# Kernel optimization log

Measured on AMD Instinct MI355X. Metric: run time of the kernel, lower is better.

The kernel has to match this reference:

```python
import jax, jax.numpy as jnp
import numpy as np

HIDDEN = 896
N_HEADS = 14
N_KV_HEADS = 2
HEAD_DIM = HIDDEN // N_HEADS  # 64
KV_GROUPS = N_HEADS // N_KV_HEADS  # 7
ROPE_THETA = 1000000.0


def rotate_half(x):
    x1, x2 = x[..., : x.shape[-1] // 2], x[..., x.shape[-1] // 2 :]
    return jnp.concatenate((-x2, x1), axis=-1)


def rope_tables(seq_len, dtype=jnp.float32):
    inv_freq = 1.0 / (ROPE_THETA ** (jnp.arange(0, HEAD_DIM, 2, dtype=jnp.float32) / HEAD_DIM))
    t = jnp.arange(seq_len, dtype=jnp.float32)
    freqs = jnp.outer(t, inv_freq)            # [S, D/2]
    emb = jnp.concatenate((freqs, freqs), -1)  # [S, D]
    return jnp.cos(emb).astype(dtype), jnp.sin(emb).astype(dtype)


def setup_inputs() -> dict:
    key = jax.random.key(0)
    ks = jax.random.split(key, 8)
    B, S = 2, 2048
    s = 0.02
    return {
        "hidden_states": jax.random.normal(ks[0], (B, S, HIDDEN), jnp.float32),
        "wq": jax.random.normal(ks[1], (HIDDEN, N_HEADS * HEAD_DIM), jnp.float32) * s,
        "bq": jnp.zeros((N_HEADS * HEAD_DIM,), jnp.float32),
        "wk": jax.random.normal(ks[2], (HIDDEN, N_KV_HEADS * HEAD_DIM), jnp.float32) * s,
        "bk": jnp.zeros((N_KV_HEADS * HEAD_DIM,), jnp.float32),
        "wv": jax.random.normal(ks[3], (HIDDEN, N_KV_HEADS * HEAD_DIM), jnp.float32) * s,
        "bv": jnp.zeros((N_KV_HEADS * HEAD_DIM,), jnp.float32),
        "wo": jax.random.normal(ks[4], (N_HEADS * HEAD_DIM, HIDDEN), jnp.float32) * s,
    }


def reference(hidden_states, wq, bq, wk, bk, wv, bv, wo):
    B, S, _ = hidden_states.shape
    q = (hidden_states @ wq + bq).reshape(B, S, N_HEADS, HEAD_DIM)
    k = (hidden_states @ wk + bk).reshape(B, S, N_KV_HEADS, HEAD_DIM)
    v = (hidden_states @ wv + bv).reshape(B, S, N_KV_HEADS, HEAD_DIM)

    cos, sin = rope_tables(S, hidden_states.dtype)
    cos, sin = cos[None, :, None, :], sin[None, :, None, :]
    q = q * cos + rotate_half(q) * sin
    k = k * cos + rotate_half(k) * sin

    # GQA broadcast: repeat kv heads to match query heads
    k = jnp.repeat(k, KV_GROUPS, axis=2)
    v = jnp.repeat(v, KV_GROUPS, axis=2)

    # [B, H, S, S]
    scores = jnp.einsum("bqhd,bkhd->bhqk", q, k) / jnp.sqrt(jnp.asarray(HEAD_DIM, hidden_states.dtype))
    mask = jnp.tril(jnp.ones((S, S), dtype=jnp.bool_))
    scores = jnp.where(mask[None, None, :, :], scores, jnp.asarray(-1e9, scores.dtype))
    attn = jax.nn.softmax(scores, axis=-1)
    out = jnp.einsum("bhqk,bkhd->bqhd", attn, v).reshape(B, S, N_HEADS * HEAD_DIM)
    return out @ wo
```

## Files before the change

kernel.cpp:

```cpp
#include <hip/hip_runtime.h>

#define HID 896
#define NQ 896
#define NKV 128
#define NQKV 1152
#define NH 14
#define NKVH 2
#define GQ 7
#define DH 64
#define SEQ 2048
#define BATCH 2
#define TOK (BATCH*SEQ)

typedef __attribute__((ext_vector_type(8))) short short8;
typedef __attribute__((ext_vector_type(4))) float f32x4;
typedef __attribute__((ext_vector_type(4))) unsigned short us4;

__device__ __forceinline__ unsigned short f2bf(float x) {
  unsigned int u = __builtin_bit_cast(unsigned int, x);
  u = (u + 0x7fffu + ((u >> 16) & 1u)) >> 16;
  return (unsigned short)u;
}
__device__ __forceinline__ float bf2f(unsigned short b) {
  return __builtin_bit_cast(float, (unsigned int)b << 16);
}
__device__ __forceinline__ f32x4 fzero4() {
  f32x4 z; z[0]=0.f; z[1]=0.f; z[2]=0.f; z[3]=0.f; return z;
}
__device__ __forceinline__ unsigned int cvt_pk_bf16(float lo, float hi) {
  unsigned int r;
  asm("v_cvt_pk_bf16_f32 %0, %1, %2" : "=v"(r) : "v"(lo), "v"(hi));
  return r;
}
__device__ __forceinline__ void gload_lds16(const unsigned short* g, unsigned short* l) {
  __builtin_amdgcn_global_load_lds(
      (const __attribute__((address_space(1))) void*)(const void*)g,
      (__attribute__((address_space(3))) void*)(void*)l, 16, 0, 0);
}

#define CVT_BLKS 3584
#define TRN_BLKS 448
#define BIAS_BLKS 5
#define TAB_BLKS 256
#define PREP_BLKS (CVT_BLKS + TRN_BLKS + BIAS_BLKS + TAB_BLKS)

__global__ void k_prep(const float* __restrict__ hs,
                       const float* __restrict__ wq, const float* __restrict__ bq,
                       const float* __restrict__ wk, const float* __restrict__ bk,
                       const float* __restrict__ wv, const float* __restrict__ bv,
                       const float* __restrict__ wo,
                       unsigned short* __restrict__ hb,
                       unsigned short* __restrict__ wqkvt,
                       unsigned short* __restrict__ wot,
                       float* __restrict__ bqkv,
                       float2* __restrict__ cs) {
  __shared__ unsigned short Ls[64*65];
  int blk = blockIdx.x, tid = threadIdx.x;
  if (blk < CVT_BLKS) {
    int i = blk*256 + tid;
    float4 v = ((const float4*)hs)[i];
    us4 o; o[0]=f2bf(v.x); o[1]=f2bf(v.y); o[2]=f2bf(v.z); o[3]=f2bf(v.w);
    ((us4*)hb)[i] = o;
    return;
  }
  blk -= CVT_BLKS;
  if (blk < TRN_BLKS) {
    const float* W; unsigned short* out; int K, N, n0, k0;
    if (blk < 196)      { W=wq; out=wqkvt;                        K=HID; N=NQ;  int t=blk;     n0=(t%14)*64; k0=(t/14)*64; }
    else if (blk < 224) { W=wk; out=wqkvt + (size_t)NQ*HID;       K=HID; N=NKV; int t=blk-196; n0=(t%2)*64;  k0=(t/2)*64; }
    else if (blk < 252) { W=wv; out=wqkvt + (size_t)(NQ+NKV)*HID; K=HID; N=NKV; int t=blk-224; n0=(t%2)*64;  k0=(t/2)*64; }
    else                { W=wo; out=wot;                          K=NQ;  N=HID; int t=blk-252; n0=(t%14)*64; k0=(t/14)*64; }
    #pragma unroll
    for (int i = 0; i < 16; ++i) {
      int idx = i*256 + tid;
      int r = idx >> 6, c = idx & 63;
      Ls[c*65 + r] = f2bf(W[(size_t)(k0 + r)*N + n0 + c]);
    }
    __syncthreads();
    #pragma unroll
    for (int i = 0; i < 16; ++i) {
      int idx = i*256 + tid;
      int r2 = idx >> 6, c2 = idx & 63;
      out[(size_t)(n0 + r2)*K + k0 + c2] = Ls[r2*65 + c2];
    }
    return;
  }
  blk -= TRN_BLKS;
  if (blk < BIAS_BLKS) {
    int i = blk*256 + tid;
    if (i < NQKV) {
      if (i < NQ) bqkv[i] = bq[i];
      else if (i < NQ + NKV) bqkv[i] = bk[i - NQ];
      else bqkv[i] = bv[i - NQ - NKV];
    }
    return;
  }
  blk -= BIAS_BLKS;
  {
    int i = blk*256 + tid;
    int s = i >> 5, dp = i & 31;
    float inv = __expf(-(float)(2*dp) * (13.815510557964274f / 64.0f));
    float f = (float)s * inv;
    cs[i] = make_float2(cosf(f), sinf(f));
  }
}

template<int OUTMODE>
__global__ __launch_bounds__(256, 3) void k_gemm_bt(
    const unsigned short* __restrict__ A,
    const unsigned short* __restrict__ Bt,
    const float* __restrict__ bias,
    const float2* __restrict__ cs,
    void* __restrict__ Cout,
    unsigned short* __restrict__ Qr,
    unsigned short* __restrict__ Kr,
    unsigned short* __restrict__ Vt,
    int M, int N, int K) {
  __shared__ unsigned short As[2][64*64];
  __shared__ unsigned short Bs[2][128*64];
  int tid = threadIdx.x;
  int lane = tid & 63, w = tid >> 6;
  int wr = w >> 1, wc = w & 1;
  int l15 = lane & 15, l4 = lane >> 4;
  int m0 = blockIdx.y * 64, n0 = blockIdx.x * 128;

  f32x4 acc[2][4];
  #pragma unroll
  for (int i = 0; i < 2; ++i)
    #pragma unroll
    for (int j = 0; j < 4; ++j) acc[i][j] = fzero4();

  auto stage = [&](int kt, int bsel) {
    int k0 = kt << 6;
    #pragma unroll
    for (int t = 0; t < 2; ++t) {
      int chunk = t*256 + w*64 + lane;
      int row = chunk >> 3, sp = chunk & 7;
      int sl = sp ^ (row & 7);
      gload_lds16(A + (size_t)(m0+row)*K + k0 + sl*8, &As[bsel][(t*256 + w*64)*8]);
    }
    #pragma unroll
    for (int t = 0; t < 4; ++t) {
      int chunk = t*256 + w*64 + lane;
      int row = chunk >> 3, sp = chunk & 7;
      int sl = sp ^ (row & 7);
      gload_lds16(Bt + (size_t)(n0+row)*K + k0 + sl*8, &Bs[bsel][(t*256 + w*64)*8]);
    }
  };

  int nkt = K >> 6;
  stage(0, 0);
  __syncthreads();
  int cur = 0;
  for (int kt = 0; kt < nkt; ++kt) {
    if (kt + 1 < nkt) stage(kt + 1, cur ^ 1);
    #pragma unroll
    for (int s = 0; s < 2; ++s) {
      short8 af[2], bfr[4];
      #pragma unroll
      for (int mi = 0; mi < 2; ++mi) {
        int row = wr*32 + mi*16 + l15;
        int slot = (s*4 + l4) ^ (row & 7);
        af[mi] = *reinterpret_cast<const short8*>(&As[cur][row*64 + slot*8]);
      }
      #pragma unroll
      for (int ni = 0; ni < 4; ++ni) {
        int row = wc*64 + ni*16 + l15;
        int slot = (s*4 + l4) ^ (row & 7);
        bfr[ni] = *reinterpret_cast<const short8*>(&Bs[cur][row*64 + slot*8]);
      }
      #pragma unroll
      for (int mi = 0; mi < 2; ++mi)
        #pragma unroll
        for (int ni = 0; ni < 4; ++ni)
          acc[mi][ni] = __builtin_amdgcn_mfma_f32_16x16x32_bf16(af[mi], bfr[ni], acc[mi][ni], 0, 0, 0);
    }
    __syncthreads();
    cur ^= 1;
  }

  if (OUTMODE == 1) {
    #pragma unroll
    for (int mi = 0; mi < 2; ++mi)
      #pragma unroll
      for (int ni = 0; ni < 4; ++ni)
        #pragma unroll
        for (int r = 0; r < 4; ++r) {
          int row = m0 + wr*32 + mi*16 + l4*4 + r;
          int col = n0 + wc*64 + ni*16 + l15;
          ((float*)Cout)[(size_t)row*N + col] = acc[mi][ni][r];
        }
    return;
  }

  int col0 = n0 + wc*64;
  if (col0 < NQ + NKV) {
    #pragma unroll
    for (int mi = 0; mi < 2; ++mi) {
      #pragma unroll
      for (int r = 0; r < 4; ++r) {
        int row = m0 + wr*32 + mi*16 + l4*4 + r;
        int b = row >> 11, s = row & 2047;
        #pragma unroll
        for (int ni = 0; ni < 2; ++ni) {
          int dp = ni*16 + l15;
          float x1 = acc[mi][ni][r]   + bias[col0 + dp];
          float x2 = acc[mi][ni+2][r] + bias[col0 + dp + 32];
          float2 c2 = cs[s*32 + dp];
          if (col0 < NQ) {
            int h = col0 >> 6;
            size_t base = ((size_t)(b*NH + h)*SEQ + s)*64;
            Qr[base + dp]      = f2bf((x1*c2.x - x2*c2.y) * 0.125f);
            Qr[base + dp + 32] = f2bf((x2*c2.x + x1*c2.y) * 0.125f);
          } else {
            int kvh = (col0 - NQ) >> 6;
            size_t base = ((size_t)(b*NKVH + kvh)*SEQ + s)*64;
            Kr[base + dp]      = f2bf(x1*c2.x - x2*c2.y);
            Kr[base + dp + 32] = f2bf(x2*c2.x + x1*c2.y);
          }
        }
      }
    }
  } else {
    int kvh = (col0 - 1024) >> 6;
    unsigned short* scr = &Bs[0][0] + w * (64*40);
    #pragma unroll
    for (int mi = 0; mi < 2; ++mi) {
      #pragma unroll
      for (int ni = 0; ni < 2; ++ni) {
        #pragma unroll
        for (int h2 = 0; h2 < 2; ++h2) {
          int dp = ni*16 + l15 + h2*32;
          float b0 = bias[col0 + dp];
          f32x4 a = acc[mi][ni + h2*2];
          uint2 pk;
          pk.x = cvt_pk_bf16(a[0] + b0, a[1] + b0);
          pk.y = cvt_pk_bf16(a[2] + b0, a[3] + b0);
          *reinterpret_cast<uint2*>(&scr[dp*40 + mi*16 + l4*4]) = pk;
        }
      }
    }
    __syncthreads();
    int srow0 = m0 + wr*32;
    int b = srow0 >> 11, s0 = srow0 & 2047;
    size_t vbase = (size_t)(b*NKVH + kvh)*64;
    #pragma unroll
    for (int p2 = 0; p2 < 4; ++p2) {
      int dp = p2*16 + (lane >> 2);
      int tok0 = (lane & 3) * 8;
      short8 v = *reinterpret_cast<const short8*>(&scr[dp*40 + tok0]);
      *reinterpret_cast<short8*>(&Vt[(vbase + dp)*SEQ + s0 + tok0]) = v;
    }
  }
}

__global__ __launch_bounds__(512, 2) void k_attn(
    const unsigned short* __restrict__ Q,
    const unsigned short* __restrict__ Kr,
    const unsigned short* __restrict__ Vt,
    unsigned short* __restrict__ Aout) {
  __shared__ __align__(16) unsigned short Kst[2][2][64*64];
  __shared__ __align__(16) unsigned short Vst[2][2][64*64];
  __shared__ __align__(16) unsigned short P_lds[8][16*64];
  int lane = threadIdx.x & 63, w = threadIdx.x >> 6;
  int grp = w >> 2, wsub = w & 3;
  int l15 = lane & 15, l4 = lane >> 4;
  int i = blockIdx.x, h = blockIdx.y, b = blockIdx.z;
  int qtH = 31 - i, qtL = i;
  int qt = grp ? qtL : qtH;
  int kvh = h / GQ;
  const unsigned short* Kb = Kr + ((size_t)(b*NKVH + kvh))*SEQ*64;
  const unsigned short* Vb = Vt + ((size_t)(b*NKVH + kvh))*64*SEQ;
  char* Pw = (char*)&P_lds[w][0];

  auto stage = [&](int slab, int bsel) {
    #pragma unroll
    for (int t = 0; t < 2; ++t) {
      int ks = slab*2 + t; if (ks > 31) ks = 31;
      int chunk = w*64 + lane;
      int row = chunk >> 3;
      int sl = (chunk & 7) ^ (row & 7);
      gload_lds16(Kb + (size_t)(ks*64 + row)*64 + sl*8, &Kst[bsel][t][chunk*8]);
      gload_lds16(Vb + (size_t)row*SEQ + ks*64 + sl*8, &Vst[bsel][t][chunk*8]);
    }
  };

  const unsigned short* Qb = Q + (((size_t)(b*NH + h))*SEQ + qt*64 + wsub*16) * 64;
  short8 qa[2];
  #pragma unroll
  for (int s = 0; s < 2; ++s)
    qa[s] = *reinterpret_cast<const short8*>(Qb + l15*64 + s*32 + l4*8);

  f32x4 acc[4];
  #pragma unroll
  for (int n = 0; n < 4; ++n) acc[n] = fzero4();
  float m_run = -__builtin_inff(), l_run = 0.0f;

  stage(0, 0);
  __syncthreads();
  int cur = 0;
  int nkt = qtH + 1;
  int nslab = (nkt + 1) >> 1;

  for (int s = 0; s < nslab; ++s) {
    if (s + 1 < nslab) stage(s + 1, cur ^ 1);
    #pragma unroll
    for (int t = 0; t < 2; ++t) {
      int ks = s*2 + t;
      if (ks <= qt) {
        const unsigned short* Ks = &Kst[cur][t][0];
        const unsigned short* Vs = &Vst[cur][t][0];
        f32x4 sa[4];
        #pragma unroll
        for (int n = 0; n < 4; ++n) sa[n] = fzero4();
        __builtin_amdgcn_s_setprio(1);
        #pragma unroll
        for (int si = 0; si < 2; ++si) {
          short8 kb[4];
          #pragma unroll
          for (int n = 0; n < 4; ++n) {
            int row = n*16 + l15;
            int slot = (si*4 + l4) ^ (row & 7);
            kb[n] = *reinterpret_cast<const short8*>(&Ks[row*64 + slot*8]);
          }
          #pragma unroll
          for (int n = 0; n < 4; ++n)
            sa[n] = __builtin_amdgcn_mfma_f32_16x16x32_bf16(kb[n], qa[si], sa[n], 0, 0, 0);
        }
        __builtin_amdgcn_s_setprio(0);
        if (ks == qt) {
          int q_glob = qt*64 + wsub*16 + l15;
          #pragma unroll
          for (int n = 0; n < 4; ++n)
            #pragma unroll
            for (int r = 0; r < 4; ++r) {
              int kpos = ks*64 + n*16 + l4*4 + r;
              if (kpos > q_glob) sa[n][r] = -1e30f;
            }
        }
        float t0 = fmaxf(fmaxf(sa[0][0],sa[0][1]), fmaxf(sa[0][2],sa[0][3]));
        float t1 = fmaxf(fmaxf(sa[1][0],sa[1][1]), fmaxf(sa[1][2],sa[1][3]));
        float t2 = fmaxf(fmaxf(sa[2][0],sa[2][1]), fmaxf(sa[2][2],sa[2][3]));
        float t3 = fmaxf(fmaxf(sa[3][0],sa[3][1]), fmaxf(sa[3][2],sa[3][3]));
        float tmax = fmaxf(fmaxf(t0,t1), fmaxf(t2,t3));
        tmax = fmaxf(tmax, __shfl_xor(tmax, 16));
        tmax = fmaxf(tmax, __shfl_xor(tmax, 32));
        float mn = fmaxf(m_run, tmax);
        float sc = __expf(m_run - mn);
        #pragma unroll
        for (int n = 0; n < 4; ++n)
          #pragma unroll
          for (int r = 0; r < 4; ++r) sa[n][r] = __expf(sa[n][r] - mn);
        float s0 = (sa[0][0]+sa[0][1]) + (sa[0][2]+sa[0][3]);
        float s1 = (sa[1][0]+sa[1][1]) + (sa[1][2]+sa[1][3]);
        float s2 = (sa[2][0]+sa[2][1]) + (sa[2][2]+sa[2][3]);
        float s3 = (sa[3][0]+sa[3][1]) + (sa[3][2]+sa[3][3]);
        float sum = (s0+s1) + (s2+s3);
        m_run = mn;
        l_run = l_run*sc + sum;
        #pragma unroll
        for (int n = 0; n < 4; ++n) acc[n] *= sc;
        #pragma unroll
        for (int n = 0; n < 4; ++n) {
          uint2 pk;
          pk.x = cvt_pk_bf16(sa[n][0], sa[n][1]);
          pk.y = cvt_pk_bf16(sa[n][2], sa[n][3]);
          int colbyte = n*32 + l4*8;
          int addr = l15*128 + ((((colbyte>>4) ^ (l15&7))) << 4) + (colbyte & 15);
          *reinterpret_cast<uint2*>(Pw + addr) = pk;
        }
        __builtin_amdgcn_s_setprio(1);
        #pragma unroll
        for (int s2i = 0; s2i < 2; ++s2i) {
          int pslot = (s2i*4 + l4) ^ (l15 & 7);
          short8 pa = *reinterpret_cast<const short8*>(Pw + l15*128 + pslot*16);
          #pragma unroll
          for (int n = 0; n < 4; ++n) {
            int row = n*16 + l15;
            int vslot = (s2i*4 + l4) ^ (row & 7);
            short8 vb = *reinterpret_cast<const short8*>(&Vs[row*64 + vslot*8]);
            acc[n] = __builtin_amdgcn_mfma_f32_16x16x32_bf16(vb, pa, acc[n], 0, 0, 0);
          }
        }
        __builtin_amdgcn_s_setprio(0);
      }
    }
    __syncthreads();
    cur ^= 1;
  }

  float lt = l_run;
  lt += __shfl_xor(lt, 16);
  lt += __shfl_xor(lt, 32);
  float inv = 1.0f / lt;
  #pragma unroll
  for (int n = 0; n < 4; ++n) {
    uint2 pk;
    pk.x = cvt_pk_bf16(acc[n][0]*inv, acc[n][1]*inv);
    pk.y = cvt_pk_bf16(acc[n][2]*inv, acc[n][3]*inv);
    int colbyte = n*32 + l4*8;
    int addr = l15*128 + ((((colbyte>>4) ^ (l15&7))) << 4) + (colbyte & 15);
    *reinterpret_cast<uint2*>(Pw + addr) = pk;
  }
  int row = lane >> 2;
  int cb0 = (lane & 3) * 32;
  #pragma unroll
  for (int it = 0; it < 2; ++it) {
    int cb = cb0 + it*16;
    int slot = (cb >> 4) ^ (row & 7);
    short8 v = *reinterpret_cast<const short8*>(Pw + row*128 + slot*16);
    size_t tok = (size_t)b*SEQ + qt*64 + wsub*16 + row;
    *reinterpret_cast<short8*>(&Aout[tok*NQ + h*64 + (cb>>1)]) = v;
  }
}

extern "C" void kernel_launch(void* const* d_in, const int* in_sizes, int n_in,
                              void* d_out, int out_size, void* d_ws, size_t ws_size,
                              hipStream_t stream) {
  const float* hs = (const float*)d_in[0];
  const float* wq = (const float*)d_in[1];
  const float* bq = (const float*)d_in[2];
  const float* wk = (const float*)d_in[3];
  const float* bk = (const float*)d_in[4];
  const float* wv = (const float*)d_in[5];
  const float* bv = (const float*)d_in[6];
  const float* wo = (const float*)d_in[7];
  float* out = (float*)d_out;

  char* p = (char*)d_ws;
  auto alloc = [&](size_t bytes) { char* r = p; p += (bytes + 255) & ~(size_t)255; return r; };
  unsigned short* hb    = (unsigned short*)alloc((size_t)TOK*HID*2);
  unsigned short* wqkvt = (unsigned short*)alloc((size_t)NQKV*HID*2);
  unsigned short* wot   = (unsigned short*)alloc((size_t)HID*NQ*2);
  float*          bqkv  = (float*)alloc(NQKV*4);
  float2*         cs    = (float2*)alloc((size_t)SEQ*32*8);
  unsigned short* q_r   = (unsigned short*)alloc((size_t)BATCH*NH*SEQ*DH*2);
  unsigned short* k_r   = (unsigned short*)alloc((size_t)BATCH*NKVH*SEQ*DH*2);
  unsigned short* v_t   = (unsigned short*)alloc((size_t)BATCH*NKVH*DH*SEQ*2);
  unsigned short* attn  = (unsigned short*)alloc((size_t)TOK*NQ*2);

  k_prep<<<PREP_BLKS, 256, 0, stream>>>(hs, wq, bq, wk, bk, wv, bv, wo,
                                        hb, wqkvt, wot, bqkv, cs);
  k_gemm_bt<0><<<dim3(NQKV/128, TOK/64), 256, 0, stream>>>(
      hb, wqkvt, bqkv, cs, nullptr, q_r, k_r, v_t, TOK, NQKV, HID);
  k_attn<<<dim3(16, NH, BATCH), 512, 0, stream>>>(q_r, k_r, v_t, attn);
  k_gemm_bt<1><<<dim3(NQ/128, TOK/64), 256, 0, stream>>>(
      attn, wot, nullptr, nullptr, out, nullptr, nullptr, nullptr, TOK, NQ, HID);
}
```

Before: 87.97 us.

## Pair adjacent query tiles per block and stage one KV tile per step

Each block now handles two adjacent query tiles (2*sb and 2*sb+1) instead of a mirrored pair (31-i and i), and blocks are launched heaviest-first. Because both wave groups need nearly the same KV range, they stay busy on almost every iteration, and the long idle tail of the light group goes away. KV staging shrinks from two-tile slabs to single-tile double buffering, which halves the shared memory used for K/V. The cost is a barrier per tile rather than per two tiles, and per-block work is now uneven, so the tail depends on launch order.

```diff
diff --git a/kernel.cpp b/kernel.cpp
--- a/kernel.cpp
+++ b/kernel.cpp
@@ -259,30 +259,26 @@
     const unsigned short* __restrict__ Kr,
     const unsigned short* __restrict__ Vt,
     unsigned short* __restrict__ Aout) {
-  __shared__ __align__(16) unsigned short Kst[2][2][64*64];
-  __shared__ __align__(16) unsigned short Vst[2][2][64*64];
+  __shared__ __align__(16) unsigned short Kst[2][64*64];
+  __shared__ __align__(16) unsigned short Vst[2][64*64];
   __shared__ __align__(16) unsigned short P_lds[8][16*64];
   int lane = threadIdx.x & 63, w = threadIdx.x >> 6;
   int grp = w >> 2, wsub = w & 3;
   int l15 = lane & 15, l4 = lane >> 4;
-  int i = blockIdx.x, h = blockIdx.y, b = blockIdx.z;
-  int qtH = 31 - i, qtL = i;
-  int qt = grp ? qtL : qtH;
+  int sb = (int)gridDim.x - 1 - (int)blockIdx.x;
+  int h = blockIdx.y, b = blockIdx.z;
+  int qt = 2*sb + grp;
   int kvh = h / GQ;
   const unsigned short* Kb = Kr + ((size_t)(b*NKVH + kvh))*SEQ*64;
   const unsigned short* Vb = Vt + ((size_t)(b*NKVH + kvh))*64*SEQ;
   char* Pw = (char*)&P_lds[w][0];
 
-  auto stage = [&](int slab, int bsel) {
-    #pragma unroll
-    for (int t = 0; t < 2; ++t) {
-      int ks = slab*2 + t; if (ks > 31) ks = 31;
-      int chunk = w*64 + lane;
-      int row = chunk >> 3;
-      int sl = (chunk & 7) ^ (row & 7);
-      gload_lds16(Kb + (size_t)(ks*64 + row)*64 + sl*8, &Kst[bsel][t][chunk*8]);
-      gload_lds16(Vb + (size_t)row*SEQ + ks*64 + sl*8, &Vst[bsel][t][chunk*8]);
-    }
+  auto stage = [&](int ks, int bsel) {
+    int chunk = w*64 + lane;
+    int row = chunk >> 3;
+    int sl = (chunk & 7) ^ (row & 7);
+    gload_lds16(Kb + (size_t)(ks*64 + row)*64 + sl*8, &Kst[bsel][chunk*8]);
+    gload_lds16(Vb + (size_t)row*SEQ + ks*64 + sl*8, &Vst[bsel][chunk*8]);
   };
 
   const unsigned short* Qb = Q + (((size_t)(b*NH + h))*SEQ + qt*64 + wsub*16) * 64;
@@ -299,91 +295,86 @@
   stage(0, 0);
   __syncthreads();
   int cur = 0;
-  int nkt = qtH + 1;
-  int nslab = (nkt + 1) >> 1;
-
-  for (int s = 0; s < nslab; ++s) {
-    if (s + 1 < nslab) stage(s + 1, cur ^ 1);
-    #pragma unroll
-    for (int t = 0; t < 2; ++t) {
-      int ks = s*2 + t;
-      if (ks <= qt) {
-        const unsigned short* Ks = &Kst[cur][t][0];
-        const unsigned short* Vs = &Vst[cur][t][0];
-        f32x4 sa[4];
-        #pragma unroll
-        for (int n = 0; n < 4; ++n) sa[n] = fzero4();
-        __builtin_amdgcn_s_setprio(1);
-        #pragma unroll
-        for (int si = 0; si < 2; ++si) {
-          short8 kb[4];
-          #pragma unroll
-          for (int n = 0; n < 4; ++n) {
-            int row = n*16 + l15;
-            int slot = (si*4 + l4) ^ (row & 7);
-            kb[n] = *reinterpret_cast<const short8*>(&Ks[row*64 + slot*8]);
-          }
-          #pragma unroll
-          for (int n = 0; n < 4; ++n)
-            sa[n] = __builtin_amdgcn_mfma_f32_16x16x32_bf16(kb[n], qa[si], sa[n], 0, 0, 0);
+  int nkt = 2*sb + 2;
+
+  for (int kt = 0; kt < nkt; ++kt) {
+    if (kt + 1 < nkt) stage(kt + 1, cur ^ 1);
+    if (kt <= qt) {
+      const unsigned short* Ks = &Kst[cur][0];
+      const unsigned short* Vs = &Vst[cur][0];
+      f32x4 sa[4];
+      #pragma unroll
+      for (int n = 0; n < 4; ++n) sa[n] = fzero4();
+      __builtin_amdgcn_s_setprio(1);
+      #pragma unroll
+      for (int si = 0; si < 2; ++si) {
+        short8 kb[4];
+        #pragma unroll
+        for (int n = 0; n < 4; ++n) {
+          int row = n*16 + l15;
+          int slot = (si*4 + l4) ^ (row & 7);
+          kb[n] = *reinterpret_cast<const short8*>(&Ks[row*64 + slot*8]);
         }
-        __builtin_amdgcn_s_setprio(0);
-        if (ks == qt) {
-          int q_glob = qt*64 + wsub*16 + l15;
-          #pragma unroll
-          for (int n = 0; n < 4; ++n)
-            #pragma unroll
-            for (int r = 0; r < 4; ++r) {
-              int kpos = ks*64 + n*16 + l4*4 + r;
-              if (kpos > q_glob) sa[n][r] = -1e30f;
-            }
-        }
-        float t0 = fmaxf(fmaxf(sa[0][0],sa[0][1]), fmaxf(sa[0][2],sa[0][3]));
-        float t1 = fmaxf(fmaxf(sa[1][0],sa[1][1]), fmaxf(sa[1][2],sa[1][3]));
-        float t2 = fmaxf(fmaxf(sa[2][0],sa[2][1]), fmaxf(sa[2][2],sa[2][3]));
-        float t3 = fmaxf(fmaxf(sa[3][0],sa[3][1]), fmaxf(sa[3][2],sa[3][3]));
-        float tmax = fmaxf(fmaxf(t0,t1), fmaxf(t2,t3));
-        tmax = fmaxf(tmax, __shfl_xor(tmax, 16));
-        tmax = fmaxf(tmax, __shfl_xor(tmax, 32));
-        float mn = fmaxf(m_run, tmax);
-        float sc = __expf(m_run - mn);
+        #pragma unroll
+        for (int n = 0; n < 4; ++n)
+          sa[n] = __builtin_amdgcn_mfma_f32_16x16x32_bf16(kb[n], qa[si], sa[n], 0, 0, 0);
+      }
+      __builtin_amdgcn_s_setprio(0);
+      if (kt == qt) {
+        int q_glob = qt*64 + wsub*16 + l15;
         #pragma unroll
         for (int n = 0; n < 4; ++n)
           #pragma unroll
-          for (int r = 0; r < 4; ++r) sa[n][r] = __expf(sa[n][r] - mn);
-        float s0 = (sa[0][0]+sa[0][1]) + (sa[0][2]+sa[0][3]);
-        float s1 = (sa[1][0]+sa[1][1]) + (sa[1][2]+sa[1][3]);
-        float s2 = (sa[2][0]+sa[2][1]) + (sa[2][2]+sa[2][3]);
-        float s3 = (sa[3][0]+sa[3][1]) + (sa[3][2]+sa[3][3]);
-        float sum = (s0+s1) + (s2+s3);
-        m_run = mn;
-        l_run = l_run*sc + sum;
-        #pragma unroll
-        for (int n = 0; n < 4; ++n) acc[n] *= sc;
+          for (int r = 0; r < 4; ++r) {
+            int kpos = kt*64 + n*16 + l4*4 + r;
+            if (kpos > q_glob) sa[n][r] = -1e30f;
+          }
+      }
+      float t0 = fmaxf(fmaxf(sa[0][0],sa[0][1]), fmaxf(sa[0][2],sa[0][3]));
+      float t1 = fmaxf(fmaxf(sa[1][0],sa[1][1]), fmaxf(sa[1][2],sa[1][3]));
+      float t2 = fmaxf(fmaxf(sa[2][0],sa[2][1]), fmaxf(sa[2][2],sa[2][3]));
+      float t3 = fmaxf(fmaxf(sa[3][0],sa[3][1]), fmaxf(sa[3][2],sa[3][3]));
+      float tmax = fmaxf(fmaxf(t0,t1), fmaxf(t2,t3));
+      tmax = fmaxf(tmax, __shfl_xor(tmax, 16));
+      tmax = fmaxf(tmax, __shfl_xor(tmax, 32));
+      float mn = fmaxf(m_run, tmax);
+      float sc = __expf(m_run - mn);
+      #pragma unroll
+      for (int n = 0; n < 4; ++n)
+        #pragma unroll
+        for (int r = 0; r < 4; ++r) sa[n][r] = __expf(sa[n][r] - mn);
+      float s0 = (sa[0][0]+sa[0][1]) + (sa[0][2]+sa[0][3]);
+      float s1 = (sa[1][0]+sa[1][1]) + (sa[1][2]+sa[1][3]);
+      float s2 = (sa[2][0]+sa[2][1]) + (sa[2][2]+sa[2][3]);
+      float s3 = (sa[3][0]+sa[3][1]) + (sa[3][2]+sa[3][3]);
+      float sum = (s0+s1) + (s2+s3);
+      m_run = mn;
+      l_run = l_run*sc + sum;
+      #pragma unroll
+      for (int n = 0; n < 4; ++n) acc[n] *= sc;
+      #pragma unroll
+      for (int n = 0; n < 4; ++n) {
+        uint2 pk;
+        pk.x = cvt_pk_bf16(sa[n][0], sa[n][1]);
+        pk.y = cvt_pk_bf16(sa[n][2], sa[n][3]);
+        int colbyte = n*32 + l4*8;
+        int addr = l15*128 + ((((colbyte>>4) ^ (l15&7))) << 4) + (colbyte & 15);
+        *reinterpret_cast<uint2*>(Pw + addr) = pk;
+      }
+      __builtin_amdgcn_s_setprio(1);
+      #pragma unroll
+      for (int s2i = 0; s2i < 2; ++s2i) {
+        int pslot = (s2i*4 + l4) ^ (l15 & 7);
+        short8 pa = *reinterpret_cast<const short8*>(Pw + l15*128 + pslot*16);
         #pragma unroll
         for (int n = 0; n < 4; ++n) {
-          uint2 pk;
-          pk.x = cvt_pk_bf16(sa[n][0], sa[n][1]);
-          pk.y = cvt_pk_bf16(sa[n][2], sa[n][3]);
-          int colbyte = n*32 + l4*8;
-          int addr = l15*128 + ((((colbyte>>4) ^ (l15&7))) << 4) + (colbyte & 15);
-          *reinterpret_cast<uint2*>(Pw + addr) = pk;
+          int row = n*16 + l15;
+          int vslot = (s2i*4 + l4) ^ (row & 7);
+          short8 vb = *reinterpret_cast<const short8*>(&Vs[row*64 + vslot*8]);
+          acc[n] = __builtin_amdgcn_mfma_f32_16x16x32_bf16(vb, pa, acc[n], 0, 0, 0);
         }
-        __builtin_amdgcn_s_setprio(1);
-        #pragma unroll
-        for (int s2i = 0; s2i < 2; ++s2i) {
-          int pslot = (s2i*4 + l4) ^ (l15 & 7);
-          short8 pa = *reinterpret_cast<const short8*>(Pw + l15*128 + pslot*16);
-          #pragma unroll
-          for (int n = 0; n < 4; ++n) {
-            int row = n*16 + l15;
-            int vslot = (s2i*4 + l4) ^ (row & 7);
-            short8 vb = *reinterpret_cast<const short8*>(&Vs[row*64 + vslot*8]);
-            acc[n] = __builtin_amdgcn_mfma_f32_16x16x32_bf16(vb, pa, acc[n], 0, 0, 0);
-          }
-        }
-        __builtin_amdgcn_s_setprio(0);
-      }
+      }
+      __builtin_amdgcn_s_setprio(0);
     }
     __syncthreads();
     cur ^= 1;
```

New measurement: 103.2 us. +17.3%, slower.

## Switch attention kernel to 32x32x16 MFMA with 32-query-row waves

Applied to the files above, without the earlier changes.

Each attention wave now handles 32 query rows with 32x32x16 bf16 MFMAs instead of 16 rows with 16x16x32, halving waves per block from 8 to 4 (256 threads). K/V staging loops over two parts per thread, and P and output LDS layouts are adapted to the 32x32 accumulator layout. This aims to raise MFMA efficiency and reduce per-row LDS fragment reads and shuffle reductions. In exchange, each wave uses more accumulator registers and a block has fewer waves to hide latency.

```diff
diff --git a/kernel.cpp b/kernel.cpp
--- a/kernel.cpp
+++ b/kernel.cpp
@@ -14,6 +14,7 @@
 
 typedef __attribute__((ext_vector_type(8))) short short8;
 typedef __attribute__((ext_vector_type(4))) float f32x4;
+typedef __attribute__((ext_vector_type(16))) float f32x16;
 typedef __attribute__((ext_vector_type(4))) unsigned short us4;
 
 __device__ __forceinline__ unsigned short f2bf(float x) {
@@ -254,17 +255,17 @@
   }
 }
 
-__global__ __launch_bounds__(512, 2) void k_attn(
+__global__ __launch_bounds__(256, 2) void k_attn(
     const unsigned short* __restrict__ Q,
     const unsigned short* __restrict__ Kr,
     const unsigned short* __restrict__ Vt,
     unsigned short* __restrict__ Aout) {
   __shared__ __align__(16) unsigned short Kst[2][2][64*64];
   __shared__ __align__(16) unsigned short Vst[2][2][64*64];
-  __shared__ __align__(16) unsigned short P_lds[8][16*64];
+  __shared__ __align__(16) unsigned short P_lds[4][32*64];
   int lane = threadIdx.x & 63, w = threadIdx.x >> 6;
-  int grp = w >> 2, wsub = w & 3;
-  int l15 = lane & 15, l4 = lane >> 4;
+  int grp = w >> 1, wsub = w & 1;
+  int l31 = lane & 31, l5 = lane >> 5;
   int i = blockIdx.x, h = blockIdx.y, b = blockIdx.z;
   int qtH = 31 - i, qtL = i;
   int qt = grp ? qtL : qtH;
@@ -277,23 +278,28 @@
     #pragma unroll
     for (int t = 0; t < 2; ++t) {
       int ks = slab*2 + t; if (ks > 31) ks = 31;
-      int chunk = w*64 + lane;
-      int row = chunk >> 3;
-      int sl = (chunk & 7) ^ (row & 7);
-      gload_lds16(Kb + (size_t)(ks*64 + row)*64 + sl*8, &Kst[bsel][t][chunk*8]);
-      gload_lds16(Vb + (size_t)row*SEQ + ks*64 + sl*8, &Vst[bsel][t][chunk*8]);
+      #pragma unroll
+      for (int part = 0; part < 2; ++part) {
+        int chunk = part*256 + threadIdx.x;
+        int row = chunk >> 3;
+        int sl = (chunk & 7) ^ (row & 7);
+        gload_lds16(Kb + (size_t)(ks*64 + row)*64 + sl*8, &Kst[bsel][t][chunk*8]);
+        gload_lds16(Vb + (size_t)row*SEQ + ks*64 + sl*8, &Vst[bsel][t][chunk*8]);
+      }
     }
   };
 
-  const unsigned short* Qb = Q + (((size_t)(b*NH + h))*SEQ + qt*64 + wsub*16) * 64;
-  short8 qa[2];
+  const unsigned short* Qb = Q + (((size_t)(b*NH + h))*SEQ + qt*64 + wsub*32) * 64;
+  short8 qa[4];
   #pragma unroll
-  for (int s = 0; s < 2; ++s)
-    qa[s] = *reinterpret_cast<const short8*>(Qb + l15*64 + s*32 + l4*8);
-
-  f32x4 acc[4];
+  for (int ds = 0; ds < 4; ++ds)
+    qa[ds] = *reinterpret_cast<const short8*>(Qb + (size_t)l31*64 + ds*16 + l5*8);
+
+  f32x16 acc[2];
   #pragma unroll
-  for (int n = 0; n < 4; ++n) acc[n] = fzero4();
+  for (int db = 0; db < 2; ++db)
+    #pragma unroll
+    for (int e = 0; e < 16; ++e) acc[db][e] = 0.0f;
   float m_run = -__builtin_inff(), l_run = 0.0f;
 
   stage(0, 0);
@@ -310,76 +316,79 @@
       if (ks <= qt) {
         const unsigned short* Ks = &Kst[cur][t][0];
         const unsigned short* Vs = &Vst[cur][t][0];
-        f32x4 sa[4];
-        #pragma unroll
-        for (int n = 0; n < 4; ++n) sa[n] = fzero4();
+        f32x16 sa[2];
+        #pragma unroll
+        for (int kb = 0; kb < 2; ++kb)
+          #pragma unroll
+          for (int e = 0; e < 16; ++e) sa[kb][e] = 0.0f;
         __builtin_amdgcn_s_setprio(1);
         #pragma unroll
-        for (int si = 0; si < 2; ++si) {
-          short8 kb[4];
-          #pragma unroll
-          for (int n = 0; n < 4; ++n) {
-            int row = n*16 + l15;
-            int slot = (si*4 + l4) ^ (row & 7);
-            kb[n] = *reinterpret_cast<const short8*>(&Ks[row*64 + slot*8]);
+        for (int ds = 0; ds < 4; ++ds) {
+          short8 kf[2];
+          #pragma unroll
+          for (int kb = 0; kb < 2; ++kb) {
+            int row = kb*32 + l31;
+            int slot = (ds*2 + l5) ^ (row & 7);
+            kf[kb] = *reinterpret_cast<const short8*>(&Ks[row*64 + slot*8]);
           }
           #pragma unroll
-          for (int n = 0; n < 4; ++n)
-            sa[n] = __builtin_amdgcn_mfma_f32_16x16x32_bf16(kb[n], qa[si], sa[n], 0, 0, 0);
+          for (int kb = 0; kb < 2; ++kb)
+            sa[kb] = __builtin_amdgcn_mfma_f32_32x32x16_bf16(kf[kb], qa[ds], sa[kb], 0, 0, 0);
         }
         __builtin_amdgcn_s_setprio(0);
         if (ks == qt) {
-          int q_glob = qt*64 + wsub*16 + l15;
-          #pragma unroll
-          for (int n = 0; n < 4; ++n)
+          int q_glob = qt*64 + wsub*32 + l31;
+          #pragma unroll
+          for (int kb = 0; kb < 2; ++kb)
             #pragma unroll
-            for (int r = 0; r < 4; ++r) {
-              int kpos = ks*64 + n*16 + l4*4 + r;
-              if (kpos > q_glob) sa[n][r] = -1e30f;
+            for (int rg = 0; rg < 16; ++rg) {
+              int kpos = ks*64 + kb*32 + (rg & 3) + 8*(rg >> 2) + 4*l5;
+              if (kpos > q_glob) sa[kb][rg] = -1e30f;
             }
         }
-        float t0 = fmaxf(fmaxf(sa[0][0],sa[0][1]), fmaxf(sa[0][2],sa[0][3]));
-        float t1 = fmaxf(fmaxf(sa[1][0],sa[1][1]), fmaxf(sa[1][2],sa[1][3]));
-        float t2 = fmaxf(fmaxf(sa[2][0],sa[2][1]), fmaxf(sa[2][2],sa[2][3]));
-        float t3 = fmaxf(fmaxf(sa[3][0],sa[3][1]), fmaxf(sa[3][2],sa[3][3]));
-        float tmax = fmaxf(fmaxf(t0,t1), fmaxf(t2,t3));
-        tmax = fmaxf(tmax, __shfl_xor(tmax, 16));
+        float tmax = -__builtin_inff();
+        #pragma unroll
+        for (int kb = 0; kb < 2; ++kb)
+          #pragma unroll
+          for (int rg = 0; rg < 16; ++rg) tmax = fmaxf(tmax, sa[kb][rg]);
         tmax = fmaxf(tmax, __shfl_xor(tmax, 32));
         float mn = fmaxf(m_run, tmax);
         float sc = __expf(m_run - mn);
-        #pragma unroll
-        for (int n = 0; n < 4; ++n)
-          #pragma unroll
-          for (int r = 0; r < 4; ++r) sa[n][r] = __expf(sa[n][r] - mn);
-        float s0 = (sa[0][0]+sa[0][1]) + (sa[0][2]+sa[0][3]);
-        float s1 = (sa[1][0]+sa[1][1]) + (sa[1][2]+sa[1][3]);
-        float s2 = (sa[2][0]+sa[2][1]) + (sa[2][2]+sa[2][3]);
-        float s3 = (sa[3][0]+sa[3][1]) + (sa[3][2]+sa[3][3]);
-        float sum = (s0+s1) + (s2+s3);
+        float sum = 0.0f;
+        #pragma unroll
+        for (int kb = 0; kb < 2; ++kb)
+          #pragma unroll
+          for (int rg = 0; rg < 16; ++rg) {
+            sa[kb][rg] = __expf(sa[kb][rg] - mn);
+            sum += sa[kb][rg];
+          }
         m_run = mn;
         l_run = l_run*sc + sum;
         #pragma unroll
-        for (int n = 0; n < 4; ++n) acc[n] *= sc;
-        #pragma unroll
-        for (int n = 0; n < 4; ++n) {
-          uint2 pk;
-          pk.x = cvt_pk_bf16(sa[n][0], sa[n][1]);
-          pk.y = cvt_pk_bf16(sa[n][2], sa[n][3]);
-          int colbyte = n*32 + l4*8;
-          int addr = l15*128 + ((((colbyte>>4) ^ (l15&7))) << 4) + (colbyte & 15);
-          *reinterpret_cast<uint2*>(Pw + addr) = pk;
-        }
+        for (int db = 0; db < 2; ++db)
+          #pragma unroll
+          for (int e = 0; e < 16; ++e) acc[db][e] *= sc;
+        #pragma unroll
+        for (int kb = 0; kb < 2; ++kb)
+          #pragma unroll
+          for (int rg = 0; rg < 4; ++rg) {
+            uint2 pk;
+            pk.x = cvt_pk_bf16(sa[kb][rg*4+0], sa[kb][rg*4+1]);
+            pk.y = cvt_pk_bf16(sa[kb][rg*4+2], sa[kb][rg*4+3]);
+            int g = rg + 4*kb;
+            *reinterpret_cast<uint2*>(Pw + l31*128 + ((g ^ (l31 & 7)) << 4) + 8*l5) = pk;
+          }
         __builtin_amdgcn_s_setprio(1);
         #pragma unroll
-        for (int s2i = 0; s2i < 2; ++s2i) {
-          int pslot = (s2i*4 + l4) ^ (l15 & 7);
-          short8 pa = *reinterpret_cast<const short8*>(Pw + l15*128 + pslot*16);
-          #pragma unroll
-          for (int n = 0; n < 4; ++n) {
-            int row = n*16 + l15;
-            int vslot = (s2i*4 + l4) ^ (row & 7);
-            short8 vb = *reinterpret_cast<const short8*>(&Vs[row*64 + vslot*8]);
-            acc[n] = __builtin_amdgcn_mfma_f32_16x16x32_bf16(vb, pa, acc[n], 0, 0, 0);
+        for (int kstep = 0; kstep < 4; ++kstep) {
+          int gp = 2*kstep + l5;
+          short8 pf = *reinterpret_cast<const short8*>(Pw + l31*128 + ((gp ^ (l31 & 7)) << 4));
+          #pragma unroll
+          for (int db = 0; db < 2; ++db) {
+            int row = db*32 + l31;
+            int slot = (2*kstep + l5) ^ (row & 7);
+            short8 vf = *reinterpret_cast<const short8*>(&Vs[row*64 + slot*8]);
+            acc[db] = __builtin_amdgcn_mfma_f32_32x32x16_bf16(vf, pf, acc[db], 0, 0, 0);
           }
         }
         __builtin_amdgcn_s_setprio(0);
@@ -389,28 +398,26 @@
     cur ^= 1;
   }
 
-  float lt = l_run;
-  lt += __shfl_xor(lt, 16);
-  lt += __shfl_xor(lt, 32);
+  float lt = l_run + __shfl_xor(l_run, 32);
   float inv = 1.0f / lt;
   #pragma unroll
-  for (int n = 0; n < 4; ++n) {
-    uint2 pk;
-    pk.x = cvt_pk_bf16(acc[n][0]*inv, acc[n][1]*inv);
-    pk.y = cvt_pk_bf16(acc[n][2]*inv, acc[n][3]*inv);
-    int colbyte = n*32 + l4*8;
-    int addr = l15*128 + ((((colbyte>>4) ^ (l15&7))) << 4) + (colbyte & 15);
-    *reinterpret_cast<uint2*>(Pw + addr) = pk;
-  }
-  int row = lane >> 2;
-  int cb0 = (lane & 3) * 32;
+  for (int db = 0; db < 2; ++db)
+    #pragma unroll
+    for (int rg = 0; rg < 4; ++rg) {
+      uint2 pk;
+      pk.x = cvt_pk_bf16(acc[db][rg*4+0]*inv, acc[db][rg*4+1]*inv);
+      pk.y = cvt_pk_bf16(acc[db][rg*4+2]*inv, acc[db][rg*4+3]*inv);
+      int g = rg + 4*db;
+      *reinterpret_cast<uint2*>(Pw + l31*128 + ((g ^ (l31 & 7)) << 4) + 8*l5) = pk;
+    }
   #pragma unroll
-  for (int it = 0; it < 2; ++it) {
-    int cb = cb0 + it*16;
-    int slot = (cb >> 4) ^ (row & 7);
-    short8 v = *reinterpret_cast<const short8*>(Pw + row*128 + slot*16);
-    size_t tok = (size_t)b*SEQ + qt*64 + wsub*16 + row;
-    *reinterpret_cast<short8*>(&Aout[tok*NQ + h*64 + (cb>>1)]) = v;
+  for (int it = 0; it < 4; ++it) {
+    int q = it*8 + (lane >> 3);
+    int c = lane & 7;
+    int slot = c ^ (q & 7);
+    short8 v = *reinterpret_cast<const short8*>(Pw + q*128 + slot*16);
+    size_t tok = (size_t)b*SEQ + qt*64 + wsub*32 + q;
+    *reinterpret_cast<short8*>(&Aout[tok*NQ + h*64 + c*8]) = v;
   }
 }
 
@@ -443,7 +450,7 @@
                                         hb, wqkvt, wot, bqkv, cs);
   k_gemm_bt<0><<<dim3(NQKV/128, TOK/64), 256, 0, stream>>>(
       hb, wqkvt, bqkv, cs, nullptr, q_r, k_r, v_t, TOK, NQKV, HID);
-  k_attn<<<dim3(16, NH, BATCH), 512, 0, stream>>>(q_r, k_r, v_t, attn);
+  k_attn<<<dim3(16, NH, BATCH), 256, 0, stream>>>(q_r, k_r, v_t, attn);
   k_gemm_bt<1><<<dim3(NQ/128, TOK/64), 256, 0, stream>>>(
       attn, wot, nullptr, nullptr, out, nullptr, nullptr, nullptr, TOK, NQ, HID);
 }
```

New measurement: 100.9 us. +14.7%, slower.

## Split heavy query tile's KV range across both warp groups with LDS merge

Applied to the files above, without the earlier changes.

Previously each block paired a heavy query tile (31-i) with a light one (i), but both warp groups walked the same shared KV slabs, so the light group sat idle for most iterations. Now group 0 handles KV tiles 0-15 of the heavy tile, and group 1 handles the remaining heavy KV tiles and then the light tile. Each group stages its own K/V, and the two partial softmax states for the heavy tile are merged through LDS at the end. The online softmax also skips rescaling unless the new max exceeds the running max by more than 8, which trades some exp-range headroom for fewer acc rescales.

```diff
diff --git a/kernel.cpp b/kernel.cpp
--- a/kernel.cpp
+++ b/kernel.cpp
@@ -267,126 +267,175 @@
   int l15 = lane & 15, l4 = lane >> 4;
   int i = blockIdx.x, h = blockIdx.y, b = blockIdx.z;
   int qtH = 31 - i, qtL = i;
-  int qt = grp ? qtL : qtH;
   int kvh = h / GQ;
   const unsigned short* Kb = Kr + ((size_t)(b*NKVH + kvh))*SEQ*64;
   const unsigned short* Vb = Vt + ((size_t)(b*NKVH + kvh))*64*SEQ;
   char* Pw = (char*)&P_lds[w][0];
 
-  auto stage = [&](int slab, int bsel) {
-    #pragma unroll
-    for (int t = 0; t < 2; ++t) {
-      int ks = slab*2 + t; if (ks > 31) ks = 31;
-      int chunk = w*64 + lane;
+  auto stage_g = [&](int ks, int bsel) {
+    int t256 = threadIdx.x & 255;
+    #pragma unroll
+    for (int part = 0; part < 2; ++part) {
+      int chunk = part*256 + t256;
       int row = chunk >> 3;
       int sl = (chunk & 7) ^ (row & 7);
-      gload_lds16(Kb + (size_t)(ks*64 + row)*64 + sl*8, &Kst[bsel][t][chunk*8]);
-      gload_lds16(Vb + (size_t)row*SEQ + ks*64 + sl*8, &Vst[bsel][t][chunk*8]);
+      gload_lds16(Kb + (size_t)(ks*64 + row)*64 + sl*8, &Kst[grp][bsel][chunk*8]);
+      gload_lds16(Vb + (size_t)row*SEQ + ks*64 + sl*8, &Vst[grp][bsel][chunk*8]);
     }
   };
 
-  const unsigned short* Qb = Q + (((size_t)(b*NH + h))*SEQ + qt*64 + wsub*16) * 64;
-  short8 qa[2];
+  const unsigned short* QbH = Q + (((size_t)(b*NH + h))*SEQ + qtH*64 + wsub*16) * 64;
+  const unsigned short* QbL = Q + (((size_t)(b*NH + h))*SEQ + qtL*64 + wsub*16) * 64;
+  short8 qaH[2], qaL[2], qac[2];
   #pragma unroll
-  for (int s = 0; s < 2; ++s)
-    qa[s] = *reinterpret_cast<const short8*>(Qb + l15*64 + s*32 + l4*8);
+  for (int si = 0; si < 2; ++si) {
+    qaH[si] = *reinterpret_cast<const short8*>(QbH + l15*64 + si*32 + l4*8);
+    qaL[si] = *reinterpret_cast<const short8*>(QbL + l15*64 + si*32 + l4*8);
+  }
+  qac[0] = qaH[0]; qac[1] = qaH[1];
 
   f32x4 acc[4];
   #pragma unroll
   for (int n = 0; n < 4; ++n) acc[n] = fzero4();
   float m_run = -__builtin_inff(), l_run = 0.0f;
-
-  stage(0, 0);
+  f32x4 aH0 = fzero4(), aH1 = fzero4(), aH2 = fzero4(), aH3 = fzero4();
+  float mH_sv = -__builtin_inff(), lH_sv = 0.0f;
+
+  int nH1 = qtH - 15;
+  stage_g(grp == 0 ? 0 : 16, 0);
   __syncthreads();
   int cur = 0;
-  int nkt = qtH + 1;
-  int nslab = (nkt + 1) >> 1;
-
-  for (int s = 0; s < nslab; ++s) {
-    if (s + 1 < nslab) stage(s + 1, cur ^ 1);
-    #pragma unroll
-    for (int t = 0; t < 2; ++t) {
-      int ks = s*2 + t;
-      if (ks <= qt) {
-        const unsigned short* Ks = &Kst[cur][t][0];
-        const unsigned short* Vs = &Vst[cur][t][0];
-        f32x4 sa[4];
-        #pragma unroll
-        for (int n = 0; n < 4; ++n) sa[n] = fzero4();
-        __builtin_amdgcn_s_setprio(1);
-        #pragma unroll
-        for (int si = 0; si < 2; ++si) {
-          short8 kb[4];
+
+  for (int it = 0; it < 17; ++it) {
+    if (grp == 0) {
+      if (it + 1 < 16) stage_g(it + 1, cur ^ 1);
+    } else {
+      int nit = it + 1;
+      if (nit < 17) stage_g(nit < nH1 ? 16 + nit : nit - nH1, cur ^ 1);
+    }
+    if (grp == 1 && it == nH1) {
+      mH_sv = m_run; lH_sv = l_run;
+      aH0 = acc[0]; aH1 = acc[1]; aH2 = acc[2]; aH3 = acc[3];
+      acc[0] = fzero4(); acc[1] = fzero4(); acc[2] = fzero4(); acc[3] = fzero4();
+      m_run = -__builtin_inff(); l_run = 0.0f;
+      qac[0] = qaL[0]; qac[1] = qaL[1];
+    }
+    bool active = (grp == 1) || (it < 16);
+    if (active) {
+      int ks, qtc;
+      if (grp == 0)        { ks = it;           qtc = qtH; }
+      else if (it < nH1)   { ks = 16 + it;      qtc = qtH; }
+      else                 { ks = it - nH1;     qtc = qtL; }
+      const unsigned short* Ks = &Kst[grp][cur][0];
+      const unsigned short* Vs = &Vst[grp][cur][0];
+      f32x4 sa[4];
+      #pragma unroll
+      for (int n = 0; n < 4; ++n) sa[n] = fzero4();
+      __builtin_amdgcn_s_setprio(1);
+      #pragma unroll
+      for (int si = 0; si < 2; ++si) {
+        short8 kb[4];
+        #pragma unroll
+        for (int n = 0; n < 4; ++n) {
+          int row = n*16 + l15;
+          int slot = (si*4 + l4) ^ (row & 7);
+          kb[n] = *reinterpret_cast<const short8*>(&Ks[row*64 + slot*8]);
+        }
+        #pragma unroll
+        for (int n = 0; n < 4; ++n)
+          sa[n] = __builtin_amdgcn_mfma_f32_16x16x32_bf16(kb[n], qac[si], sa[n], 0, 0, 0);
+      }
+      __builtin_amdgcn_s_setprio(0);
+      if (ks == qtc) {
+        int q_glob = qtc*64 + wsub*16 + l15;
+        #pragma unroll
+        for (int n = 0; n < 4; ++n)
           #pragma unroll
-          for (int n = 0; n < 4; ++n) {
-            int row = n*16 + l15;
-            int slot = (si*4 + l4) ^ (row & 7);
-            kb[n] = *reinterpret_cast<const short8*>(&Ks[row*64 + slot*8]);
+          for (int r = 0; r < 4; ++r) {
+            int kpos = ks*64 + n*16 + l4*4 + r;
+            if (kpos > q_glob) sa[n][r] = -1e30f;
           }
-          #pragma unroll
-          for (int n = 0; n < 4; ++n)
-            sa[n] = __builtin_amdgcn_mfma_f32_16x16x32_bf16(kb[n], qa[si], sa[n], 0, 0, 0);
-        }
-        __builtin_amdgcn_s_setprio(0);
-        if (ks == qt) {
-          int q_glob = qt*64 + wsub*16 + l15;
-          #pragma unroll
-          for (int n = 0; n < 4; ++n)
-            #pragma unroll
-            for (int r = 0; r < 4; ++r) {
-              int kpos = ks*64 + n*16 + l4*4 + r;
-              if (kpos > q_glob) sa[n][r] = -1e30f;
-            }
-        }
-        float t0 = fmaxf(fmaxf(sa[0][0],sa[0][1]), fmaxf(sa[0][2],sa[0][3]));
-        float t1 = fmaxf(fmaxf(sa[1][0],sa[1][1]), fmaxf(sa[1][2],sa[1][3]));
-        float t2 = fmaxf(fmaxf(sa[2][0],sa[2][1]), fmaxf(sa[2][2],sa[2][3]));
-        float t3 = fmaxf(fmaxf(sa[3][0],sa[3][1]), fmaxf(sa[3][2],sa[3][3]));
-        float tmax = fmaxf(fmaxf(t0,t1), fmaxf(t2,t3));
-        tmax = fmaxf(tmax, __shfl_xor(tmax, 16));
-        tmax = fmaxf(tmax, __shfl_xor(tmax, 32));
+      }
+      float t0 = fmaxf(fmaxf(sa[0][0],sa[0][1]), fmaxf(sa[0][2],sa[0][3]));
+      float t1 = fmaxf(fmaxf(sa[1][0],sa[1][1]), fmaxf(sa[1][2],sa[1][3]));
+      float t2 = fmaxf(fmaxf(sa[2][0],sa[2][1]), fmaxf(sa[2][2],sa[2][3]));
+      float t3 = fmaxf(fmaxf(sa[3][0],sa[3][1]), fmaxf(sa[3][2],sa[3][3]));
+      float tmax = fmaxf(fmaxf(t0,t1), fmaxf(t2,t3));
+      tmax = fmaxf(tmax, __shfl_xor(tmax, 16));
+      tmax = fmaxf(tmax, __shfl_xor(tmax, 32));
+      if (!__all(tmax <= m_run + 8.0f)) {
         float mn = fmaxf(m_run, tmax);
         float sc = __expf(m_run - mn);
-        #pragma unroll
-        for (int n = 0; n < 4; ++n)
-          #pragma unroll
-          for (int r = 0; r < 4; ++r) sa[n][r] = __expf(sa[n][r] - mn);
-        float s0 = (sa[0][0]+sa[0][1]) + (sa[0][2]+sa[0][3]);
-        float s1 = (sa[1][0]+sa[1][1]) + (sa[1][2]+sa[1][3]);
-        float s2 = (sa[2][0]+sa[2][1]) + (sa[2][2]+sa[2][3]);
-        float s3 = (sa[3][0]+sa[3][1]) + (sa[3][2]+sa[3][3]);
-        float sum = (s0+s1) + (s2+s3);
+        l_run *= sc;
+        #pragma unroll
+        for (int n = 0; n < 4; ++n) acc[n] *= sc;
         m_run = mn;
-        l_run = l_run*sc + sum;
-        #pragma unroll
-        for (int n = 0; n < 4; ++n) acc[n] *= sc;
+      }
+      #pragma unroll
+      for (int n = 0; n < 4; ++n)
+        #pragma unroll
+        for (int r = 0; r < 4; ++r) sa[n][r] = __expf(sa[n][r] - m_run);
+      float s0 = (sa[0][0]+sa[0][1]) + (sa[0][2]+sa[0][3]);
+      float s1 = (sa[1][0]+sa[1][1]) + (sa[1][2]+sa[1][3]);
+      float s2 = (sa[2][0]+sa[2][1]) + (sa[2][2]+sa[2][3]);
+      float s3 = (sa[3][0]+sa[3][1]) + (sa[3][2]+sa[3][3]);
+      l_run += (s0+s1) + (s2+s3);
+      #pragma unroll
+      for (int n = 0; n < 4; ++n) {
+        uint2 pk;
+        pk.x = cvt_pk_bf16(sa[n][0], sa[n][1]);
+        pk.y = cvt_pk_bf16(sa[n][2], sa[n][3]);
+        int colbyte = n*32 + l4*8;
+        int addr = l15*128 + ((((colbyte>>4) ^ (l15&7))) << 4) + (colbyte & 15);
+        *reinterpret_cast<uint2*>(Pw + addr) = pk;
+      }
+      __builtin_amdgcn_s_setprio(1);
+      #pragma unroll
+      for (int s2i = 0; s2i < 2; ++s2i) {
+        int pslot = (s2i*4 + l4) ^ (l15 & 7);
+        short8 pa = *reinterpret_cast<const short8*>(Pw + l15*128 + pslot*16);
         #pragma unroll
         for (int n = 0; n < 4; ++n) {
-          uint2 pk;
-          pk.x = cvt_pk_bf16(sa[n][0], sa[n][1]);
-          pk.y = cvt_pk_bf16(sa[n][2], sa[n][3]);
-          int colbyte = n*32 + l4*8;
-          int addr = l15*128 + ((((colbyte>>4) ^ (l15&7))) << 4) + (colbyte & 15);
-          *reinterpret_cast<uint2*>(Pw + addr) = pk;
+          int row = n*16 + l15;
+          int vslot = (s2i*4 + l4) ^ (row & 7);
+          short8 vb = *reinterpret_cast<const short8*>(&Vs[row*64 + vslot*8]);
+          acc[n] = __builtin_amdgcn_mfma_f32_16x16x32_bf16(vb, pa, acc[n], 0, 0, 0);
         }
-        __builtin_amdgcn_s_setprio(1);
-        #pragma unroll
-        for (int s2i = 0; s2i < 2; ++s2i) {
-          int pslot = (s2i*4 + l4) ^ (l15 & 7);
-          short8 pa = *reinterpret_cast<const short8*>(Pw + l15*128 + pslot*16);
-          #pragma unroll
-          for (int n = 0; n < 4; ++n) {
-            int row = n*16 + l15;
-            int vslot = (s2i*4 + l4) ^ (row & 7);
-            short8 vb = *reinterpret_cast<const short8*>(&Vs[row*64 + vslot*8]);
-            acc[n] = __builtin_amdgcn_mfma_f32_16x16x32_bf16(vb, pa, acc[n], 0, 0, 0);
-          }
-        }
-        __builtin_amdgcn_s_setprio(0);
-      }
+      }
+      __builtin_amdgcn_s_setprio(0);
     }
     __syncthreads();
     cur ^= 1;
+  }
+
+  float* cb = (float*)&Kst[0][0][0];
+  int cidx = (wsub*64 + lane) * 21;
+  if (grp == 1) {
+    cb[cidx+0] = mH_sv;
+    cb[cidx+1] = lH_sv;
+    #pragma unroll
+    for (int r = 0; r < 4; ++r) {
+      cb[cidx+2+r]  = aH0[r];
+      cb[cidx+6+r]  = aH1[r];
+      cb[cidx+10+r] = aH2[r];
+      cb[cidx+14+r] = aH3[r];
+    }
+  }
+  __syncthreads();
+  int qt_out;
+  if (grp == 0) {
+    float m1 = cb[cidx+0], l1 = cb[cidx+1];
+    float m = fmaxf(m_run, m1);
+    float e0 = __expf(m_run - m), e1 = __expf(m1 - m);
+    l_run = l_run*e0 + l1*e1;
+    #pragma unroll
+    for (int n = 0; n < 4; ++n)
+      #pragma unroll
+      for (int r = 0; r < 4; ++r)
+        acc[n][r] = acc[n][r]*e0 + cb[cidx+2+n*4+r]*e1;
+    qt_out = qtH;
+  } else {
+    qt_out = qtL;
   }
 
   float lt = l_run;
@@ -406,11 +455,11 @@
   int cb0 = (lane & 3) * 32;
   #pragma unroll
   for (int it = 0; it < 2; ++it) {
-    int cb = cb0 + it*16;
-    int slot = (cb >> 4) ^ (row & 7);
+    int cbyte = cb0 + it*16;
+    int slot = (cbyte >> 4) ^ (row & 7);
     short8 v = *reinterpret_cast<const short8*>(Pw + row*128 + slot*16);
-    size_t tok = (size_t)b*SEQ + qt*64 + wsub*16 + row;
-    *reinterpret_cast<short8*>(&Aout[tok*NQ + h*64 + (cb>>1)]) = v;
+    size_t tok = (size_t)b*SEQ + qt_out*64 + wsub*16 + row;
+    *reinterpret_cast<short8*>(&Aout[tok*NQ + h*64 + (cbyte>>1)]) = v;
   }
 }
 
```

New measurement: 99.95 us. 13.6% more time.
